# Kernel tuning notes

Hardware: AMD Instinct MI355X
Metric: run time of the kernel (lower is better)

## Reference

```python
import jax, jax.numpy as jnp
import numpy as np

B, F, C, NS, P, N = 256, 2048, 16384, 65536, 8, 32
T, W_BU, W_H, P_MARGIN, N_MARGIN = 1.0, 1.0, 10.0, 0.1, 0.1


def setup_inputs() -> dict:
    key = jax.random.key(0)
    ks = jax.random.split(key, 8)
    inputs = jax.random.normal(ks[0], (B, F), jnp.float32)
    targets = jax.random.randint(ks[1], (B,), 0, C)
    # batch global indices: unique (original .item() assumes a single match)
    indexs = jax.random.permutation(ks[2], NS)[:B].astype(jnp.int64) if False else jax.random.permutation(ks[2], jnp.arange(NS))[:B]
    # positive candidates drawn from in-batch indices so they are found in `indexs`
    pos_sel = jax.random.randint(ks[3], (B, P), 0, B)
    ppairs = indexs[pos_sel]
    # negative candidates: arbitrary global indices (mostly not in batch)
    npairs = jax.random.randint(ks[4], (B, N), 0, NS)
    all_label_to_clusterid = jax.random.randint(ks[5], (NS,), 0, C)
    V = jax.random.normal(ks[6], (C, F), jnp.float32)
    V = V / jnp.linalg.norm(V, axis=1, keepdims=True)  # bank rows are L2-normalized by the update rule
    return {"inputs": inputs, "targets": targets, "ppairs": ppairs, "npairs": npairs,
            "indexs": indexs, "all_label_to_clusterid": all_label_to_clusterid, "V": V, "epoch": 1}


def _forward(inputs, targets, ppairs, npairs, indexs, all_label_to_clusterid, V, epoch):
    # Exclusive branch: logits against the memory bank (V treated as constant)
    outputs = (inputs @ V.T) * T  # [B, C]
    logp = jax.nn.log_softmax(outputs, axis=1)
    bu_loss = -jnp.mean(jnp.take_along_axis(logp, targets[:, None], axis=1))

    # ms_loss (use_prior=True, use_table=True)
    ni = inputs / jnp.linalg.norm(inputs, axis=1, keepdims=True)
    sims = ni @ ni.T          # [B, B]
    tsims = ni @ V.T          # [B, C]

    # positives found in the batch: (ppair == indexs).nonzero()
    mp = ppairs[:, :, None] == indexs[None, None, :]        # [B, P, B]
    found_p = jnp.any(mp, axis=2)
    idx_p = jnp.argmax(mp, axis=2)
    psim_b = jnp.take_along_axis(sims, idx_p, axis=1)       # [B, P]
    mask_pb = found_p & (ppairs >= 0)
    # table positive: tsims[i, target] appended if nonzero
    tp = jnp.take_along_axis(tsims, targets[:, None], axis=1)  # [B, 1]
    mask_tp = tp != 0
    psims = jnp.concatenate([psim_b, tp], axis=1)           # [B, P+1]
    pmask = jnp.concatenate([mask_pb, mask_tp], axis=1)

    # negatives found in the batch
    mn = npairs[:, :, None] == indexs[None, None, :]        # [B, N, B]
    found_n = jnp.any(mn, axis=2)
    idx_n = jnp.argmax(mn, axis=2)
    nsim_b = jnp.take_along_axis(sims, idx_n, axis=1)       # [B, N]
    mask_nb = found_n & (npairs >= 0)
    # table negative appended for EVERY npair (indent level in original): tsims[i, clusterid[npair]]
    ncid = all_label_to_clusterid[jnp.clip(npairs, 0, None)]
    tn = jnp.take_along_axis(tsims, ncid, axis=1)           # [B, N]
    mask_tn = (npairs >= 0) & (tn != 0)
    nsims = jnp.concatenate([nsim_b, tn], axis=1)           # [B, 2N]
    nmask = jnp.concatenate([mask_nb, mask_tn], axis=1)

    # thresholds: max(nsims) or -3 (+p_margin); min(psims) or 3 (-n_margin)
    p_thrd = jnp.where(jnp.any(nmask, 1), jnp.max(jnp.where(nmask, nsims, -jnp.inf), 1), -3.0) + P_MARGIN
    n_thrd = jnp.where(jnp.any(pmask, 1), jnp.min(jnp.where(pmask, psims, jnp.inf), 1), 3.0) - N_MARGIN

    hp = pmask & (psims < p_thrd[:, None])
    hn = nmask & (nsims > n_thrd[:, None]) & (nsims < 0.999999)

    hp_sum = jnp.sum(jnp.where(hp, jnp.exp(-2.0 * (psims - 0.5)), 0.0))
    hn_sum = jnp.sum(jnp.where(hn, jnp.exp(50.0 * (nsims - 0.5)), 0.0))
    hp_loss = jnp.where(jnp.any(hp), 0.5 * jnp.log1p(hp_sum), 0.0)
    hn_loss = jnp.where(jnp.any(hn), (1.0 / 50.0) * jnp.log1p(hn_sum), 0.0)
    # original builds hpsims/hnsims with torch.tensor(...), which DETACHES them
    h_loss = jax.lax.stop_gradient(hp_loss + hn_loss)

    loss = W_BU * bu_loss + W_H * h_loss
    return loss, outputs


def reference(inputs, targets, ppairs, npairs, indexs, all_label_to_clusterid, V, epoch):
    return _forward(inputs, targets, ppairs, npairs, indexs, all_label_to_clusterid, V, epoch)
```

## Files before the change

### kernel.cpp

```cpp
#include <hip/hip_runtime.h>
#include <hip/hip_bf16.h>
#include <math.h>

#define B_SZ 256
#define F_SZ 2048
#define C_SZ 16384
#define P_SZ 8
#define N_SZ 32
#define NTILE 256

typedef __bf16 bf16x8 __attribute__((ext_vector_type(8)));
typedef float f32x4 __attribute__((ext_vector_type(4)));
typedef unsigned short us8 __attribute__((ext_vector_type(8)));

typedef __attribute__((address_space(3))) unsigned int lds_u32;
typedef __attribute__((address_space(1))) const unsigned int glb_u32;

#define WAITCNT_VM4   0x0F74
#define WAITCNT_VM0   0x0F70
#define WAITCNT_LGKM0 0xC07F

__device__ __forceinline__ unsigned short f2bf(float x) {
    union { float f; unsigned int u; } v; v.f = x;
    unsigned int r = v.u + 0x7FFFu + ((v.u >> 16) & 1u);
    return (unsigned short)(r >> 16);
}

__global__ __launch_bounds__(256) void prep_kernel(const float* __restrict__ inputs,
                                                   unsigned short* __restrict__ Abf,
                                                   float* __restrict__ norms) {
    const int row = blockIdx.x;
    const int tid = threadIdx.x;
    const float* rp = inputs + (size_t)row * F_SZ + tid * 8;
    float4 v0 = *(const float4*)(rp);
    float4 v1 = *(const float4*)(rp + 4);
    us8 o;
    o[0]=f2bf(v0.x); o[1]=f2bf(v0.y); o[2]=f2bf(v0.z); o[3]=f2bf(v0.w);
    o[4]=f2bf(v1.x); o[5]=f2bf(v1.y); o[6]=f2bf(v1.z); o[7]=f2bf(v1.w);
    *(us8*)(Abf + (size_t)row * F_SZ + tid * 8) = o;
    float ss = v0.x*v0.x + v0.y*v0.y + v0.z*v0.z + v0.w*v0.w
             + v1.x*v1.x + v1.y*v1.y + v1.z*v1.z + v1.w*v1.w;
    __shared__ float red[256];
    red[tid] = ss; __syncthreads();
    for (int s = 128; s > 0; s >>= 1) { if (tid < s) red[tid] += red[tid+s]; __syncthreads(); }
    if (tid == 0) norms[row] = sqrtf(red[0]);
}

#define BM 128
#define BN 64
#define BK 64
#define BPAD 72
#define KITERS (F_SZ / BK)

__global__ __launch_bounds__(256, 2) void gemm_kernel(const unsigned short* __restrict__ Abf,
                                                      const float* __restrict__ V,
                                                      float* __restrict__ Cout,
                                                      float* __restrict__ pmax,
                                                      float* __restrict__ psum) {
    __shared__ unsigned short As[3][BM * BK];
    __shared__ unsigned short Bs[2][BN * BPAD];
    __shared__ float sm[BM * 2], ss2[BM * 2];

    const int tid = threadIdx.x;
    const int lane = tid & 63;
    const int wid = tid >> 6;
    const int wm = wid >> 1, wn = wid & 1;
    const int q = lane >> 4, l16 = lane & 15;

    const int bid = blockIdx.x;
    const int mhalf = (bid >> 3) & 1;
    const int slab  = (bid & 7) | ((bid >> 4) << 3);
    const int bm0 = mhalf * BM;
    const int bn0 = slab * BN;

    f32x4 acc[4][2];
    #pragma unroll
    for (int i = 0; i < 4; i++)
        #pragma unroll
        for (int j = 0; j < 2; j++) acc[i][j] = (f32x4){0.f, 0.f, 0.f, 0.f};

    const int arow = tid >> 3;
    const int akc = (tid & 7) ^ (arow & 7);
    const unsigned short* AgBase = Abf + (size_t)(bm0 + arow) * F_SZ + akc * 8;

    const int bcol = tid >> 2, bseg = tid & 3;
    const float* BgBase = V + (size_t)(bn0 + bcol) * F_SZ + bseg * 16;
    const int bsoff = bcol * BPAD + bseg * 16;

    float4 b0, b1, b2, b3;

    auto issueA = [&](int ring, int k0) {
        #pragma unroll
        for (int j = 0; j < 4; ++j) {
            __builtin_amdgcn_global_load_lds(
                (glb_u32*)(AgBase + (size_t)j * 32 * F_SZ + k0),
                (lds_u32*)&As[ring][(j * 256 + wid * 64) * 8],
                16, 0, 0);
        }
    };
    auto loadB = [&](int k0) {
        b0 = *(const float4*)(BgBase + k0);
        b1 = *(const float4*)(BgBase + k0 + 4);
        b2 = *(const float4*)(BgBase + k0 + 8);
        b3 = *(const float4*)(BgBase + k0 + 12);
    };
    auto writeB = [&](int buf) {
        us8 w0, w1;
        w0[0]=f2bf(b0.x); w0[1]=f2bf(b0.y); w0[2]=f2bf(b0.z); w0[3]=f2bf(b0.w);
        w0[4]=f2bf(b1.x); w0[5]=f2bf(b1.y); w0[6]=f2bf(b1.z); w0[7]=f2bf(b1.w);
        w1[0]=f2bf(b2.x); w1[1]=f2bf(b2.y); w1[2]=f2bf(b2.z); w1[3]=f2bf(b2.w);
        w1[4]=f2bf(b3.x); w1[5]=f2bf(b3.y); w1[6]=f2bf(b3.z); w1[7]=f2bf(b3.w);
        *(us8*)&Bs[buf][bsoff] = w0;
        *(us8*)&Bs[buf][bsoff + 8] = w1;
    };
    auto compute = [&](int ring, int buf) {
        #pragma unroll
        for (int ks = 0; ks < 2; ++ks) {
            bf16x8 af[4], bfv[2];
            const int kc = ks * 4 + q;
            #pragma unroll
            for (int mi = 0; mi < 4; ++mi) {
                const int row = wm * 64 + mi * 16 + l16;
                af[mi] = *(const bf16x8*)&As[ring][row * 64 + (kc ^ (row & 7)) * 8];
            }
            #pragma unroll
            for (int ni = 0; ni < 2; ++ni) {
                const int col = wn * 32 + ni * 16 + l16;
                bfv[ni] = *(const bf16x8*)&Bs[buf][col * BPAD + ks * 32 + q * 8];
            }
            #pragma unroll
            for (int mi = 0; mi < 4; ++mi)
                #pragma unroll
                for (int ni = 0; ni < 2; ++ni)
                    acc[mi][ni] = __builtin_amdgcn_mfma_f32_16x16x32_bf16(af[mi], bfv[ni], acc[mi][ni], 0, 0, 0);
        }
    };

    issueA(0, 0);
    issueA(1, BK);
    loadB(0);
    __builtin_amdgcn_s_waitcnt(WAITCNT_VM0);
    writeB(0);
    __syncthreads();

    int cur = 0;
    int nxt2 = 2;
    #pragma unroll 1
    for (int it = 0; it < KITERS; ++it) {
        if (it + 1 < KITERS) loadB((it + 1) * BK);
        if (it + 2 < KITERS) issueA(nxt2, (it + 2) * BK);
        compute(cur, it & 1);
        if (it + 2 < KITERS)      __builtin_amdgcn_s_waitcnt(WAITCNT_VM4);
        else if (it + 1 < KITERS) __builtin_amdgcn_s_waitcnt(WAITCNT_VM0);
        if (it + 1 < KITERS) {
            writeB((it + 1) & 1);
            __builtin_amdgcn_s_waitcnt(WAITCNT_LGKM0);
            __builtin_amdgcn_s_barrier();
        }
        cur  = (cur == 2) ? 0 : cur + 1;
        nxt2 = (nxt2 == 2) ? 0 : nxt2 + 1;
    }

    #pragma unroll
    for (int mi = 0; mi < 4; ++mi) {
        const int r0 = bm0 + wm * 64 + mi * 16 + q * 4;
        #pragma unroll
        for (int ni = 0; ni < 2; ++ni) {
            const int c0 = bn0 + wn * 32 + ni * 16 + l16;
            #pragma unroll
            for (int r = 0; r < 4; ++r)
                Cout[(size_t)(r0 + r) * C_SZ + c0] = acc[mi][ni][r];
        }
    }

    #pragma unroll
    for (int mi = 0; mi < 4; ++mi) {
        #pragma unroll
        for (int r = 0; r < 4; ++r) {
            float mloc = fmaxf(acc[mi][0][r], acc[mi][1][r]);
            #pragma unroll
            for (int off = 1; off < 16; off <<= 1)
                mloc = fmaxf(mloc, __shfl_xor(mloc, off, 64));
            float sloc = __expf(acc[mi][0][r] - mloc) + __expf(acc[mi][1][r] - mloc);
            #pragma unroll
            for (int off = 1; off < 16; off <<= 1)
                sloc += __shfl_xor(sloc, off, 64);
            if (l16 == 0) {
                const int lrow = wm * 64 + mi * 16 + q * 4 + r;
                sm[lrow * 2 + wn] = mloc;
                ss2[lrow * 2 + wn] = sloc;
            }
        }
    }
    __syncthreads();
    if (tid < BM) {
        float m1 = sm[tid * 2], s1 = ss2[tid * 2];
        float m2 = sm[tid * 2 + 1], s2 = ss2[tid * 2 + 1];
        float nm = fmaxf(m1, m2);
        float s = s1 * __expf(m1 - nm) + s2 * __expf(m2 - nm);
        pmax[(bm0 + tid) * NTILE + slab] = nm;
        psum[(bm0 + tid) * NTILE + slab] = s;
    }
}

__global__ __launch_bounds__(256) void softmax_combine_kernel(
    const float* __restrict__ pmax, const float* __restrict__ psum,
    const float* __restrict__ outputs, const int* __restrict__ targets,
    float* __restrict__ bu_part)
{
    const int row = blockIdx.x;
    const int tid = threadIdx.x;
    __shared__ float rm[256], rs[256];
    rm[tid] = pmax[row * NTILE + tid];
    rs[tid] = psum[row * NTILE + tid];
    __syncthreads();
    for (int s = 128; s > 0; s >>= 1) {
        if (tid < s) {
            float a = rm[tid], sa = rs[tid];
            float b = rm[tid + s], sb = rs[tid + s];
            float nn = fmaxf(a, b);
            rs[tid] = sa * __expf(a - nn) + sb * __expf(b - nn);
            rm[tid] = nn;
        }
        __syncthreads();
    }
    if (tid == 0) {
        float logZ = rm[0] + logf(rs[0]);
        bu_part[row] = -(outputs[(size_t)row * C_SZ + targets[row]] - logZ);
    }
}

__global__ __launch_bounds__(256) void pairs_kernel(
    const float* __restrict__ inputs, const int* __restrict__ targets,
    const int* __restrict__ ppairs, const int* __restrict__ npairs,
    const int* __restrict__ indexs, const int* __restrict__ cluster,
    const float* __restrict__ outputs, const float* __restrict__ norms,
    float* __restrict__ hp_part, float* __restrict__ hn_part,
    int* __restrict__ flag_part)
{
    const int i = blockIdx.x;
    const int tid = threadIdx.x;
    __shared__ int idxbuf[B_SZ];
    __shared__ int pj[P_SZ];
    __shared__ int nj[N_SZ];
    __shared__ float simp[P_SZ];
    __shared__ float simn[N_SZ];
    __shared__ float tnv[N_SZ];
    __shared__ float s_tp;

    idxbuf[tid] = indexs[tid];
    __syncthreads();

    const float* row = outputs + (size_t)i * C_SZ;
    const float ni_norm = norms[i];

    if (tid < P_SZ) {
        int pp = ppairs[i * P_SZ + tid];
        int f = -1;
        if (pp >= 0) for (int j = 0; j < B_SZ; j++) if (idxbuf[j] == pp) { f = j; break; }
        pj[tid] = f;
    } else if (tid < P_SZ + N_SZ) {
        int t = tid - P_SZ;
        int np = npairs[i * N_SZ + t];
        int f = -1;
        if (np >= 0) for (int j = 0; j < B_SZ; j++) if (idxbuf[j] == np) { f = j; break; }
        nj[t] = f;
        int cid = cluster[np < 0 ? 0 : np];
        tnv[t] = row[cid] / ni_norm;
    }
    if (tid == P_SZ + N_SZ) s_tp = row[targets[i]] / ni_norm;
    __syncthreads();

    const int lane = tid & 63, wv = tid >> 6;
    for (int qq = wv; qq < P_SZ + N_SZ; qq += 4) {
        int j = (qq < P_SZ) ? pj[qq] : nj[qq - P_SZ];
        float s = 0.f;
        if (j >= 0) {
            const float* xi = inputs + (size_t)i * F_SZ;
            const float* xj = inputs + (size_t)j * F_SZ;
            float d = 0.f;
            for (int k = lane; k < F_SZ; k += 64) d += xi[k] * xj[k];
            for (int off = 32; off > 0; off >>= 1) d += __shfl_down(d, off);
            s = d / (ni_norm * norms[j]);
        }
        if (lane == 0) { if (qq < P_SZ) simp[qq] = s; else simn[qq - P_SZ] = s; }
    }
    __syncthreads();

    if (tid == 0) {
        float psims[P_SZ + 1]; bool pmask[P_SZ + 1];
        for (int p = 0; p < P_SZ; p++) {
            int pp = ppairs[i * P_SZ + p];
            pmask[p] = (pj[p] >= 0) && (pp >= 0);
            psims[p] = simp[p];
        }
        psims[P_SZ] = s_tp; pmask[P_SZ] = (s_tp != 0.0f);

        float nsims[2 * N_SZ]; bool nmask[2 * N_SZ];
        for (int t = 0; t < N_SZ; t++) {
            int np = npairs[i * N_SZ + t];
            nmask[t] = (nj[t] >= 0) && (np >= 0);
            nsims[t] = simn[t];
            nsims[N_SZ + t] = tnv[t];
            nmask[N_SZ + t] = (np >= 0) && (tnv[t] != 0.0f);
        }
        bool anyp = false, anyn = false;
        float maxn = -INFINITY, minp = INFINITY;
        for (int t = 0; t < 2 * N_SZ; t++) if (nmask[t]) { anyn = true; maxn = fmaxf(maxn, nsims[t]); }
        for (int p = 0; p < P_SZ + 1; p++) if (pmask[p]) { anyp = true; minp = fminf(minp, psims[p]); }
        float p_thrd = (anyn ? maxn : -3.0f) + 0.1f;
        float n_thrd = (anyp ? minp : 3.0f) - 0.1f;
        float hps = 0.f, hns = 0.f; int fl = 0;
        for (int p = 0; p < P_SZ + 1; p++)
            if (pmask[p] && psims[p] < p_thrd) { fl |= 1; hps += expf(-2.0f * (psims[p] - 0.5f)); }
        for (int t = 0; t < 2 * N_SZ; t++)
            if (nmask[t] && nsims[t] > n_thrd && nsims[t] < 0.999999f) { fl |= 2; hns += expf(50.0f * (nsims[t] - 0.5f)); }
        hp_part[i] = hps; hn_part[i] = hns; flag_part[i] = fl;
    }
}

__global__ __launch_bounds__(256) void finalize_kernel(
    const float* __restrict__ bu_part, const float* __restrict__ hp_part,
    const float* __restrict__ hn_part, const int* __restrict__ flag_part,
    float* __restrict__ d_out)
{
    __shared__ float r1[256], r2[256], r3[256];
    __shared__ int rf[256];
    const int tid = threadIdx.x;
    r1[tid] = bu_part[tid]; r2[tid] = hp_part[tid]; r3[tid] = hn_part[tid]; rf[tid] = flag_part[tid];
    __syncthreads();
    for (int s = 128; s > 0; s >>= 1) {
        if (tid < s) { r1[tid] += r1[tid+s]; r2[tid] += r2[tid+s]; r3[tid] += r3[tid+s]; rf[tid] |= rf[tid+s]; }
        __syncthreads();
    }
    if (tid == 0) {
        float bu = r1[0] / (float)B_SZ;
        float hp_loss = (rf[0] & 1) ? 0.5f * log1pf(r2[0]) : 0.0f;
        float hn_loss = (rf[0] & 2) ? (1.0f / 50.0f) * log1pf(r3[0]) : 0.0f;
        d_out[0] = 1.0f * bu + 10.0f * (hp_loss + hn_loss);
    }
}

extern "C" void kernel_launch(void* const* d_in, const int* in_sizes, int n_in,
                              void* d_out, int out_size, void* d_ws, size_t ws_size,
                              hipStream_t stream) {
    const float* inputs  = (const float*)d_in[0];
    const int*   targets = (const int*)d_in[1];
    const int*   ppairs  = (const int*)d_in[2];
    const int*   npairs  = (const int*)d_in[3];
    const int*   indexs  = (const int*)d_in[4];
    const int*   cluster = (const int*)d_in[5];
    const float* V       = (const float*)d_in[6];
    float* out = (float*)d_out;

    char* ws = (char*)d_ws;
    unsigned short* Abf = (unsigned short*)ws;
    float* norms   = (float*)(ws + (size_t)B_SZ * F_SZ * 2);
    float* bu_part = norms + B_SZ;
    float* hp_part = bu_part + B_SZ;
    float* hn_part = hp_part + B_SZ;
    int*   flag_part = (int*)(hn_part + B_SZ);
    float* pmax = (float*)(flag_part + B_SZ);
    float* psum = pmax + (size_t)B_SZ * NTILE;

    prep_kernel<<<B_SZ, 256, 0, stream>>>(inputs, Abf, norms);
    gemm_kernel<<<512, 256, 0, stream>>>(Abf, V, out + 1, pmax, psum);
    softmax_combine_kernel<<<B_SZ, 256, 0, stream>>>(pmax, psum, out + 1, targets, bu_part);
    pairs_kernel<<<B_SZ, 256, 0, stream>>>(inputs, targets, ppairs, npairs, indexs,
                                           cluster, out + 1, norms,
                                           hp_part, hn_part, flag_part);
    finalize_kernel<<<1, 256, 0, stream>>>(bu_part, hp_part, hn_part, flag_part, out);
}
```

Before: 302.7 us.

## Deepen B prefetch to two stages and fuse softmax combine into pairs kernel

The GEMM's fp32 V loads now go into two alternating register sets, so the load for k-step it+2 is issued two iterations ahead. The wait count is relaxed to allow 8 outstanding loads, which hides more global latency behind the MFMA work. The separate softmax_combine kernel is removed and its log-sum-exp reduction is folded into pairs_kernel, saving one launch. The cost is more live registers in the GEMM, which could reduce occupancy, plus extra shared memory and barriers in pairs_kernel.

```diff
diff --git a/kernel.cpp b/kernel.cpp
--- a/kernel.cpp
+++ b/kernel.cpp
@@ -16,7 +16,7 @@
 typedef __attribute__((address_space(3))) unsigned int lds_u32;
 typedef __attribute__((address_space(1))) const unsigned int glb_u32;
 
-#define WAITCNT_VM4   0x0F74
+#define WAITCNT_VM8   0x0F78
 #define WAITCNT_VM0   0x0F70
 #define WAITCNT_LGKM0 0xC07F
 
@@ -87,7 +87,8 @@
     const float* BgBase = V + (size_t)(bn0 + bcol) * F_SZ + bseg * 16;
     const int bsoff = bcol * BPAD + bseg * 16;
 
-    float4 b0, b1, b2, b3;
+    float4 p0, p1, p2, p3;
+    float4 q0, q1, q2, q3;
 
     auto issueA = [&](int ring, int k0) {
         #pragma unroll
@@ -98,20 +99,35 @@
                 16, 0, 0);
         }
     };
-    auto loadB = [&](int k0) {
-        b0 = *(const float4*)(BgBase + k0);
-        b1 = *(const float4*)(BgBase + k0 + 4);
-        b2 = *(const float4*)(BgBase + k0 + 8);
-        b3 = *(const float4*)(BgBase + k0 + 12);
-    };
-    auto writeB = [&](int buf) {
+    auto loadBp = [&](int k0) {
+        p0 = *(const float4*)(BgBase + k0);
+        p1 = *(const float4*)(BgBase + k0 + 4);
+        p2 = *(const float4*)(BgBase + k0 + 8);
+        p3 = *(const float4*)(BgBase + k0 + 12);
+    };
+    auto loadBq = [&](int k0) {
+        q0 = *(const float4*)(BgBase + k0);
+        q1 = *(const float4*)(BgBase + k0 + 4);
+        q2 = *(const float4*)(BgBase + k0 + 8);
+        q3 = *(const float4*)(BgBase + k0 + 12);
+    };
+    auto writeBp = [&]() {
         us8 w0, w1;
-        w0[0]=f2bf(b0.x); w0[1]=f2bf(b0.y); w0[2]=f2bf(b0.z); w0[3]=f2bf(b0.w);
-        w0[4]=f2bf(b1.x); w0[5]=f2bf(b1.y); w0[6]=f2bf(b1.z); w0[7]=f2bf(b1.w);
-        w1[0]=f2bf(b2.x); w1[1]=f2bf(b2.y); w1[2]=f2bf(b2.z); w1[3]=f2bf(b2.w);
-        w1[4]=f2bf(b3.x); w1[5]=f2bf(b3.y); w1[6]=f2bf(b3.z); w1[7]=f2bf(b3.w);
-        *(us8*)&Bs[buf][bsoff] = w0;
-        *(us8*)&Bs[buf][bsoff + 8] = w1;
+        w0[0]=f2bf(p0.x); w0[1]=f2bf(p0.y); w0[2]=f2bf(p0.z); w0[3]=f2bf(p0.w);
+        w0[4]=f2bf(p1.x); w0[5]=f2bf(p1.y); w0[6]=f2bf(p1.z); w0[7]=f2bf(p1.w);
+        w1[0]=f2bf(p2.x); w1[1]=f2bf(p2.y); w1[2]=f2bf(p2.z); w1[3]=f2bf(p2.w);
+        w1[4]=f2bf(p3.x); w1[5]=f2bf(p3.y); w1[6]=f2bf(p3.z); w1[7]=f2bf(p3.w);
+        *(us8*)&Bs[0][bsoff] = w0;
+        *(us8*)&Bs[0][bsoff + 8] = w1;
+    };
+    auto writeBq = [&]() {
+        us8 w0, w1;
+        w0[0]=f2bf(q0.x); w0[1]=f2bf(q0.y); w0[2]=f2bf(q0.z); w0[3]=f2bf(q0.w);
+        w0[4]=f2bf(q1.x); w0[5]=f2bf(q1.y); w0[6]=f2bf(q1.z); w0[7]=f2bf(q1.w);
+        w1[0]=f2bf(q2.x); w1[1]=f2bf(q2.y); w1[2]=f2bf(q2.z); w1[3]=f2bf(q2.w);
+        w1[4]=f2bf(q3.x); w1[5]=f2bf(q3.y); w1[6]=f2bf(q3.z); w1[7]=f2bf(q3.w);
+        *(us8*)&Bs[1][bsoff] = w0;
+        *(us8*)&Bs[1][bsoff + 8] = w1;
     };
     auto compute = [&](int ring, int buf) {
         #pragma unroll
@@ -137,23 +153,29 @@
     };
 
     issueA(0, 0);
+    loadBp(0);
     issueA(1, BK);
-    loadB(0);
-    __builtin_amdgcn_s_waitcnt(WAITCNT_VM0);
-    writeB(0);
-    __syncthreads();
+    loadBq(BK);
+    __builtin_amdgcn_s_waitcnt(WAITCNT_VM8);
+    writeBp();
+    __builtin_amdgcn_s_waitcnt(WAITCNT_LGKM0);
+    __builtin_amdgcn_s_barrier();
 
     int cur = 0;
     int nxt2 = 2;
     #pragma unroll 1
     for (int it = 0; it < KITERS; ++it) {
-        if (it + 1 < KITERS) loadB((it + 1) * BK);
-        if (it + 2 < KITERS) issueA(nxt2, (it + 2) * BK);
+        if (it + 2 < KITERS) {
+            issueA(nxt2, (it + 2) * BK);
+            if (!(it & 1)) loadBp((it + 2) * BK);
+            else           loadBq((it + 2) * BK);
+        }
         compute(cur, it & 1);
-        if (it + 2 < KITERS)      __builtin_amdgcn_s_waitcnt(WAITCNT_VM4);
+        if (it + 2 < KITERS)      __builtin_amdgcn_s_waitcnt(WAITCNT_VM8);
         else if (it + 1 < KITERS) __builtin_amdgcn_s_waitcnt(WAITCNT_VM0);
         if (it + 1 < KITERS) {
-            writeB((it + 1) & 1);
+            if (!(it & 1)) writeBq();
+            else           writeBp();
             __builtin_amdgcn_s_waitcnt(WAITCNT_LGKM0);
             __builtin_amdgcn_s_barrier();
         }
@@ -203,38 +225,13 @@
     }
 }
 
-__global__ __launch_bounds__(256) void softmax_combine_kernel(
-    const float* __restrict__ pmax, const float* __restrict__ psum,
-    const float* __restrict__ outputs, const int* __restrict__ targets,
-    float* __restrict__ bu_part)
-{
-    const int row = blockIdx.x;
-    const int tid = threadIdx.x;
-    __shared__ float rm[256], rs[256];
-    rm[tid] = pmax[row * NTILE + tid];
-    rs[tid] = psum[row * NTILE + tid];
-    __syncthreads();
-    for (int s = 128; s > 0; s >>= 1) {
-        if (tid < s) {
-            float a = rm[tid], sa = rs[tid];
-            float b = rm[tid + s], sb = rs[tid + s];
-            float nn = fmaxf(a, b);
-            rs[tid] = sa * __expf(a - nn) + sb * __expf(b - nn);
-            rm[tid] = nn;
-        }
-        __syncthreads();
-    }
-    if (tid == 0) {
-        float logZ = rm[0] + logf(rs[0]);
-        bu_part[row] = -(outputs[(size_t)row * C_SZ + targets[row]] - logZ);
-    }
-}
-
 __global__ __launch_bounds__(256) void pairs_kernel(
     const float* __restrict__ inputs, const int* __restrict__ targets,
     const int* __restrict__ ppairs, const int* __restrict__ npairs,
     const int* __restrict__ indexs, const int* __restrict__ cluster,
     const float* __restrict__ outputs, const float* __restrict__ norms,
+    const float* __restrict__ pmax, const float* __restrict__ psum,
+    float* __restrict__ bu_part,
     float* __restrict__ hp_part, float* __restrict__ hn_part,
     int* __restrict__ flag_part)
 {
@@ -247,12 +244,30 @@
     __shared__ float simn[N_SZ];
     __shared__ float tnv[N_SZ];
     __shared__ float s_tp;
+    __shared__ float rm[256], rs[256];
 
     idxbuf[tid] = indexs[tid];
-    __syncthreads();
+    rm[tid] = pmax[i * NTILE + tid];
+    rs[tid] = psum[i * NTILE + tid];
+    __syncthreads();
+    for (int s = 128; s > 0; s >>= 1) {
+        if (tid < s) {
+            float a = rm[tid], sa = rs[tid];
+            float b = rm[tid + s], sb = rs[tid + s];
+            float nn = fmaxf(a, b);
+            rs[tid] = sa * __expf(a - nn) + sb * __expf(b - nn);
+            rm[tid] = nn;
+        }
+        __syncthreads();
+    }
 
     const float* row = outputs + (size_t)i * C_SZ;
     const float ni_norm = norms[i];
+
+    if (tid == 0) {
+        float logZ = rm[0] + logf(rs[0]);
+        bu_part[i] = -(row[targets[i]] - logZ);
+    }
 
     if (tid < P_SZ) {
         int pp = ppairs[i * P_SZ + tid];
@@ -365,9 +380,8 @@
 
     prep_kernel<<<B_SZ, 256, 0, stream>>>(inputs, Abf, norms);
     gemm_kernel<<<512, 256, 0, stream>>>(Abf, V, out + 1, pmax, psum);
-    softmax_combine_kernel<<<B_SZ, 256, 0, stream>>>(pmax, psum, out + 1, targets, bu_part);
     pairs_kernel<<<B_SZ, 256, 0, stream>>>(inputs, targets, ppairs, npairs, indexs,
-                                           cluster, out + 1, norms,
-                                           hp_part, hn_part, flag_part);
+                                           cluster, out + 1, norms, pmax, psum,
+                                           bu_part, hp_part, hn_part, flag_part);
     finalize_kernel<<<1, 256, 0, stream>>>(bu_part, hp_part, hn_part, flag_part, out);
 }
```

Result: no change. 300.1 us (-0.9%).

## Pre-convert V to bf16 and stream both GEMM operands via direct LDS loads

Applied to the files above, without the earlier changes.

Adds a bulk fp32-to-bf16 conversion of the memory bank V in the prep kernel, so the GEMM can load both A and B tiles with asynchronous global-to-LDS loads into a triple-buffered swizzled ring. This removes the register staging, in-loop conversion and extra LDS writes for B. The softmax-combine kernel is merged into the pairs kernel to drop a launch. The cost is an extra full pass over V that reads fp32 and writes bf16 each call, plus more workspace.

```diff
diff --git a/kernel.cpp b/kernel.cpp
--- a/kernel.cpp
+++ b/kernel.cpp
@@ -16,9 +16,8 @@
 typedef __attribute__((address_space(3))) unsigned int lds_u32;
 typedef __attribute__((address_space(1))) const unsigned int glb_u32;
 
-#define WAITCNT_VM4   0x0F74
+#define WAITCNT_VM6   0x0F76
 #define WAITCNT_VM0   0x0F70
-#define WAITCNT_LGKM0 0xC07F
 
 __device__ __forceinline__ unsigned short f2bf(float x) {
     union { float f; unsigned int u; } v; v.f = x;
@@ -26,11 +25,29 @@
     return (unsigned short)(r >> 16);
 }
 
+#define VCONV_BLKS 4096
+
 __global__ __launch_bounds__(256) void prep_kernel(const float* __restrict__ inputs,
+                                                   const float* __restrict__ V,
                                                    unsigned short* __restrict__ Abf,
+                                                   unsigned short* __restrict__ Vbf,
                                                    float* __restrict__ norms) {
-    const int row = blockIdx.x;
     const int tid = threadIdx.x;
+    if (blockIdx.x < VCONV_BLKS) {
+        const size_t base = (size_t)blockIdx.x * 8192 + tid * 8;
+        #pragma unroll
+        for (int c = 0; c < 4; ++c) {
+            const float* rp = V + base + c * 2048;
+            float4 v0 = *(const float4*)(rp);
+            float4 v1 = *(const float4*)(rp + 4);
+            us8 o;
+            o[0]=f2bf(v0.x); o[1]=f2bf(v0.y); o[2]=f2bf(v0.z); o[3]=f2bf(v0.w);
+            o[4]=f2bf(v1.x); o[5]=f2bf(v1.y); o[6]=f2bf(v1.z); o[7]=f2bf(v1.w);
+            *(us8*)(Vbf + base + c * 2048) = o;
+        }
+        return;
+    }
+    const int row = blockIdx.x - VCONV_BLKS;
     const float* rp = inputs + (size_t)row * F_SZ + tid * 8;
     float4 v0 = *(const float4*)(rp);
     float4 v1 = *(const float4*)(rp + 4);
@@ -49,16 +66,15 @@
 #define BM 128
 #define BN 64
 #define BK 64
-#define BPAD 72
 #define KITERS (F_SZ / BK)
 
 __global__ __launch_bounds__(256, 2) void gemm_kernel(const unsigned short* __restrict__ Abf,
-                                                      const float* __restrict__ V,
+                                                      const unsigned short* __restrict__ Vbf,
                                                       float* __restrict__ Cout,
                                                       float* __restrict__ pmax,
                                                       float* __restrict__ psum) {
     __shared__ unsigned short As[3][BM * BK];
-    __shared__ unsigned short Bs[2][BN * BPAD];
+    __shared__ unsigned short Bs[3][BN * BK];
     __shared__ float sm[BM * 2], ss2[BM * 2];
 
     const int tid = threadIdx.x;
@@ -79,17 +95,12 @@
         #pragma unroll
         for (int j = 0; j < 2; j++) acc[i][j] = (f32x4){0.f, 0.f, 0.f, 0.f};
 
-    const int arow = tid >> 3;
-    const int akc = (tid & 7) ^ (arow & 7);
-    const unsigned short* AgBase = Abf + (size_t)(bm0 + arow) * F_SZ + akc * 8;
-
-    const int bcol = tid >> 2, bseg = tid & 3;
-    const float* BgBase = V + (size_t)(bn0 + bcol) * F_SZ + bseg * 16;
-    const int bsoff = bcol * BPAD + bseg * 16;
-
-    float4 b0, b1, b2, b3;
-
-    auto issueA = [&](int ring, int k0) {
+    const int srow = tid >> 3;
+    const int skc = (tid & 7) ^ (srow & 7);
+    const unsigned short* AgBase = Abf + (size_t)(bm0 + srow) * F_SZ + skc * 8;
+    const unsigned short* BgBase = Vbf + (size_t)(bn0 + srow) * F_SZ + skc * 8;
+
+    auto issueTile = [&](int ring, int k0) {
         #pragma unroll
         for (int j = 0; j < 4; ++j) {
             __builtin_amdgcn_global_load_lds(
@@ -97,23 +108,15 @@
                 (lds_u32*)&As[ring][(j * 256 + wid * 64) * 8],
                 16, 0, 0);
         }
+        #pragma unroll
+        for (int j = 0; j < 2; ++j) {
+            __builtin_amdgcn_global_load_lds(
+                (glb_u32*)(BgBase + (size_t)j * 32 * F_SZ + k0),
+                (lds_u32*)&Bs[ring][(j * 256 + wid * 64) * 8],
+                16, 0, 0);
+        }
     };
-    auto loadB = [&](int k0) {
-        b0 = *(const float4*)(BgBase + k0);
-        b1 = *(const float4*)(BgBase + k0 + 4);
-        b2 = *(const float4*)(BgBase + k0 + 8);
-        b3 = *(const float4*)(BgBase + k0 + 12);
-    };
-    auto writeB = [&](int buf) {
-        us8 w0, w1;
-        w0[0]=f2bf(b0.x); w0[1]=f2bf(b0.y); w0[2]=f2bf(b0.z); w0[3]=f2bf(b0.w);
-        w0[4]=f2bf(b1.x); w0[5]=f2bf(b1.y); w0[6]=f2bf(b1.z); w0[7]=f2bf(b1.w);
-        w1[0]=f2bf(b2.x); w1[1]=f2bf(b2.y); w1[2]=f2bf(b2.z); w1[3]=f2bf(b2.w);
-        w1[4]=f2bf(b3.x); w1[5]=f2bf(b3.y); w1[6]=f2bf(b3.z); w1[7]=f2bf(b3.w);
-        *(us8*)&Bs[buf][bsoff] = w0;
-        *(us8*)&Bs[buf][bsoff + 8] = w1;
-    };
-    auto compute = [&](int ring, int buf) {
+    auto compute = [&](int ring) {
         #pragma unroll
         for (int ks = 0; ks < 2; ++ks) {
             bf16x8 af[4], bfv[2];
@@ -126,7 +129,7 @@
             #pragma unroll
             for (int ni = 0; ni < 2; ++ni) {
                 const int col = wn * 32 + ni * 16 + l16;
-                bfv[ni] = *(const bf16x8*)&Bs[buf][col * BPAD + ks * 32 + q * 8];
+                bfv[ni] = *(const bf16x8*)&Bs[ring][col * 64 + (kc ^ (col & 7)) * 8];
             }
             #pragma unroll
             for (int mi = 0; mi < 4; ++mi)
@@ -136,27 +139,20 @@
         }
     };
 
-    issueA(0, 0);
-    issueA(1, BK);
-    loadB(0);
-    __builtin_amdgcn_s_waitcnt(WAITCNT_VM0);
-    writeB(0);
-    __syncthreads();
+    issueTile(0, 0);
+    issueTile(1, BK);
+    __builtin_amdgcn_s_waitcnt(WAITCNT_VM6);
+    __builtin_amdgcn_s_barrier();
 
     int cur = 0;
     int nxt2 = 2;
     #pragma unroll 1
     for (int it = 0; it < KITERS; ++it) {
-        if (it + 1 < KITERS) loadB((it + 1) * BK);
-        if (it + 2 < KITERS) issueA(nxt2, (it + 2) * BK);
-        compute(cur, it & 1);
-        if (it + 2 < KITERS)      __builtin_amdgcn_s_waitcnt(WAITCNT_VM4);
+        if (it + 2 < KITERS) issueTile(nxt2, (it + 2) * BK);
+        compute(cur);
+        if (it + 2 < KITERS)      __builtin_amdgcn_s_waitcnt(WAITCNT_VM6);
         else if (it + 1 < KITERS) __builtin_amdgcn_s_waitcnt(WAITCNT_VM0);
-        if (it + 1 < KITERS) {
-            writeB((it + 1) & 1);
-            __builtin_amdgcn_s_waitcnt(WAITCNT_LGKM0);
-            __builtin_amdgcn_s_barrier();
-        }
+        if (it + 1 < KITERS) __builtin_amdgcn_s_barrier();
         cur  = (cur == 2) ? 0 : cur + 1;
         nxt2 = (nxt2 == 2) ? 0 : nxt2 + 1;
     }
@@ -203,38 +199,13 @@
     }
 }
 
-__global__ __launch_bounds__(256) void softmax_combine_kernel(
-    const float* __restrict__ pmax, const float* __restrict__ psum,
-    const float* __restrict__ outputs, const int* __restrict__ targets,
-    float* __restrict__ bu_part)
-{
-    const int row = blockIdx.x;
-    const int tid = threadIdx.x;
-    __shared__ float rm[256], rs[256];
-    rm[tid] = pmax[row * NTILE + tid];
-    rs[tid] = psum[row * NTILE + tid];
-    __syncthreads();
-    for (int s = 128; s > 0; s >>= 1) {
-        if (tid < s) {
-            float a = rm[tid], sa = rs[tid];
-            float b = rm[tid + s], sb = rs[tid + s];
-            float nn = fmaxf(a, b);
-            rs[tid] = sa * __expf(a - nn) + sb * __expf(b - nn);
-            rm[tid] = nn;
-        }
-        __syncthreads();
-    }
-    if (tid == 0) {
-        float logZ = rm[0] + logf(rs[0]);
-        bu_part[row] = -(outputs[(size_t)row * C_SZ + targets[row]] - logZ);
-    }
-}
-
 __global__ __launch_bounds__(256) void pairs_kernel(
     const float* __restrict__ inputs, const int* __restrict__ targets,
     const int* __restrict__ ppairs, const int* __restrict__ npairs,
     const int* __restrict__ indexs, const int* __restrict__ cluster,
     const float* __restrict__ outputs, const float* __restrict__ norms,
+    const float* __restrict__ pmax, const float* __restrict__ psum,
+    float* __restrict__ bu_part,
     float* __restrict__ hp_part, float* __restrict__ hn_part,
     int* __restrict__ flag_part)
 {
@@ -247,12 +218,30 @@
     __shared__ float simn[N_SZ];
     __shared__ float tnv[N_SZ];
     __shared__ float s_tp;
+    __shared__ float rm[256], rs[256];
 
     idxbuf[tid] = indexs[tid];
-    __syncthreads();
+    rm[tid] = pmax[i * NTILE + tid];
+    rs[tid] = psum[i * NTILE + tid];
+    __syncthreads();
+    for (int s = 128; s > 0; s >>= 1) {
+        if (tid < s) {
+            float a = rm[tid], sa = rs[tid];
+            float b = rm[tid + s], sb = rs[tid + s];
+            float nn = fmaxf(a, b);
+            rs[tid] = sa * __expf(a - nn) + sb * __expf(b - nn);
+            rm[tid] = nn;
+        }
+        __syncthreads();
+    }
 
     const float* row = outputs + (size_t)i * C_SZ;
     const float ni_norm = norms[i];
+
+    if (tid == 0) {
+        float logZ = rm[0] + logf(rs[0]);
+        bu_part[i] = -(row[targets[i]] - logZ);
+    }
 
     if (tid < P_SZ) {
         int pp = ppairs[i * P_SZ + tid];
@@ -354,8 +343,9 @@
     float* out = (float*)d_out;
 
     char* ws = (char*)d_ws;
-    unsigned short* Abf = (unsigned short*)ws;
-    float* norms   = (float*)(ws + (size_t)B_SZ * F_SZ * 2);
+    unsigned short* Vbf = (unsigned short*)ws;
+    unsigned short* Abf = Vbf + (size_t)C_SZ * F_SZ;
+    float* norms   = (float*)(Abf + (size_t)B_SZ * F_SZ);
     float* bu_part = norms + B_SZ;
     float* hp_part = bu_part + B_SZ;
     float* hn_part = hp_part + B_SZ;
@@ -363,11 +353,10 @@
     float* pmax = (float*)(flag_part + B_SZ);
     float* psum = pmax + (size_t)B_SZ * NTILE;
 
-    prep_kernel<<<B_SZ, 256, 0, stream>>>(inputs, Abf, norms);
-    gemm_kernel<<<512, 256, 0, stream>>>(Abf, V, out + 1, pmax, psum);
-    softmax_combine_kernel<<<B_SZ, 256, 0, stream>>>(pmax, psum, out + 1, targets, bu_part);
+    prep_kernel<<<VCONV_BLKS + B_SZ, 256, 0, stream>>>(inputs, V, Abf, Vbf, norms);
+    gemm_kernel<<<512, 256, 0, stream>>>(Abf, Vbf, out + 1, pmax, psum);
     pairs_kernel<<<B_SZ, 256, 0, stream>>>(inputs, targets, ppairs, npairs, indexs,
-                                           cluster, out + 1, norms,
-                                           hp_part, hn_part, flag_part);
+                                           cluster, out + 1, norms, pmax, psum,
+                                           bu_part, hp_part, hn_part, flag_part);
     finalize_kernel<<<1, 256, 0, stream>>>(bu_part, hp_part, hn_part, flag_part, out);
 }
```

After: 326.0 us. +7.7%, slower.

## Cover all batch rows per GEMM block and fold softmax combine into pairs

Applied to the files above, without the earlier changes.

The GEMM block tile grows from 128 to all 256 batch rows, with 512 threads and one block per 64-column slab of V. Each fp32 V slab is now loaded and converted to bf16 once rather than once per M-half. The separate softmax_combine kernel is removed and its log-sum-exp reduction moved into pairs_kernel, saving a launch. In exchange the grid is only 256 blocks at one block per CU with a larger LDS footprint, which reduces latency hiding.

```diff
diff --git a/kernel.cpp b/kernel.cpp
--- a/kernel.cpp
+++ b/kernel.cpp
@@ -46,13 +46,13 @@
     if (tid == 0) norms[row] = sqrtf(red[0]);
 }
 
-#define BM 128
+#define BM 256
 #define BN 64
 #define BK 64
 #define BPAD 72
 #define KITERS (F_SZ / BK)
 
-__global__ __launch_bounds__(256, 2) void gemm_kernel(const unsigned short* __restrict__ Abf,
+__global__ __launch_bounds__(512, 1) void gemm_kernel(const unsigned short* __restrict__ Abf,
                                                       const float* __restrict__ V,
                                                       float* __restrict__ Cout,
                                                       float* __restrict__ pmax,
@@ -67,10 +67,7 @@
     const int wm = wid >> 1, wn = wid & 1;
     const int q = lane >> 4, l16 = lane & 15;
 
-    const int bid = blockIdx.x;
-    const int mhalf = (bid >> 3) & 1;
-    const int slab  = (bid & 7) | ((bid >> 4) << 3);
-    const int bm0 = mhalf * BM;
+    const int slab = blockIdx.x;
     const int bn0 = slab * BN;
 
     f32x4 acc[4][2];
@@ -79,39 +76,34 @@
         #pragma unroll
         for (int j = 0; j < 2; j++) acc[i][j] = (f32x4){0.f, 0.f, 0.f, 0.f};
 
-    const int arow = tid >> 3;
-    const int akc = (tid & 7) ^ (arow & 7);
-    const unsigned short* AgBase = Abf + (size_t)(bm0 + arow) * F_SZ + akc * 8;
-
-    const int bcol = tid >> 2, bseg = tid & 3;
-    const float* BgBase = V + (size_t)(bn0 + bcol) * F_SZ + bseg * 16;
-    const int bsoff = bcol * BPAD + bseg * 16;
-
-    float4 b0, b1, b2, b3;
+    const int srow = tid >> 3;
+    const int skc = (tid & 7) ^ (srow & 7);
+    const unsigned short* AgBase = Abf + (size_t)srow * F_SZ + skc * 8;
+
+    const int bcol = tid >> 3, bseg = tid & 7;
+    const float* BgBase = V + (size_t)(bn0 + bcol) * F_SZ + bseg * 8;
+    const int bsoff = bcol * BPAD + bseg * 8;
+
+    float4 b0, b1;
 
     auto issueA = [&](int ring, int k0) {
         #pragma unroll
         for (int j = 0; j < 4; ++j) {
             __builtin_amdgcn_global_load_lds(
-                (glb_u32*)(AgBase + (size_t)j * 32 * F_SZ + k0),
-                (lds_u32*)&As[ring][(j * 256 + wid * 64) * 8],
+                (glb_u32*)(AgBase + (size_t)j * 64 * F_SZ + k0),
+                (lds_u32*)&As[ring][(j * 512 + tid) * 8],
                 16, 0, 0);
         }
     };
     auto loadB = [&](int k0) {
         b0 = *(const float4*)(BgBase + k0);
         b1 = *(const float4*)(BgBase + k0 + 4);
-        b2 = *(const float4*)(BgBase + k0 + 8);
-        b3 = *(const float4*)(BgBase + k0 + 12);
     };
     auto writeB = [&](int buf) {
-        us8 w0, w1;
-        w0[0]=f2bf(b0.x); w0[1]=f2bf(b0.y); w0[2]=f2bf(b0.z); w0[3]=f2bf(b0.w);
-        w0[4]=f2bf(b1.x); w0[5]=f2bf(b1.y); w0[6]=f2bf(b1.z); w0[7]=f2bf(b1.w);
-        w1[0]=f2bf(b2.x); w1[1]=f2bf(b2.y); w1[2]=f2bf(b2.z); w1[3]=f2bf(b2.w);
-        w1[4]=f2bf(b3.x); w1[5]=f2bf(b3.y); w1[6]=f2bf(b3.z); w1[7]=f2bf(b3.w);
-        *(us8*)&Bs[buf][bsoff] = w0;
-        *(us8*)&Bs[buf][bsoff + 8] = w1;
+        us8 w;
+        w[0]=f2bf(b0.x); w[1]=f2bf(b0.y); w[2]=f2bf(b0.z); w[3]=f2bf(b0.w);
+        w[4]=f2bf(b1.x); w[5]=f2bf(b1.y); w[6]=f2bf(b1.z); w[7]=f2bf(b1.w);
+        *(us8*)&Bs[buf][bsoff] = w;
     };
     auto compute = [&](int ring, int buf) {
         #pragma unroll
@@ -137,11 +129,12 @@
     };
 
     issueA(0, 0);
+    loadB(0);
     issueA(1, BK);
-    loadB(0);
-    __builtin_amdgcn_s_waitcnt(WAITCNT_VM0);
+    __builtin_amdgcn_s_waitcnt(WAITCNT_VM4);
     writeB(0);
-    __syncthreads();
+    __builtin_amdgcn_s_waitcnt(WAITCNT_LGKM0);
+    __builtin_amdgcn_s_barrier();
 
     int cur = 0;
     int nxt2 = 2;
@@ -163,7 +156,7 @@
 
     #pragma unroll
     for (int mi = 0; mi < 4; ++mi) {
-        const int r0 = bm0 + wm * 64 + mi * 16 + q * 4;
+        const int r0 = wm * 64 + mi * 16 + q * 4;
         #pragma unroll
         for (int ni = 0; ni < 2; ++ni) {
             const int c0 = bn0 + wn * 32 + ni * 16 + l16;
@@ -198,35 +191,8 @@
         float m2 = sm[tid * 2 + 1], s2 = ss2[tid * 2 + 1];
         float nm = fmaxf(m1, m2);
         float s = s1 * __expf(m1 - nm) + s2 * __expf(m2 - nm);
-        pmax[(bm0 + tid) * NTILE + slab] = nm;
-        psum[(bm0 + tid) * NTILE + slab] = s;
-    }
-}
-
-__global__ __launch_bounds__(256) void softmax_combine_kernel(
-    const float* __restrict__ pmax, const float* __restrict__ psum,
-    const float* __restrict__ outputs, const int* __restrict__ targets,
-    float* __restrict__ bu_part)
-{
-    const int row = blockIdx.x;
-    const int tid = threadIdx.x;
-    __shared__ float rm[256], rs[256];
-    rm[tid] = pmax[row * NTILE + tid];
-    rs[tid] = psum[row * NTILE + tid];
-    __syncthreads();
-    for (int s = 128; s > 0; s >>= 1) {
-        if (tid < s) {
-            float a = rm[tid], sa = rs[tid];
-            float b = rm[tid + s], sb = rs[tid + s];
-            float nn = fmaxf(a, b);
-            rs[tid] = sa * __expf(a - nn) + sb * __expf(b - nn);
-            rm[tid] = nn;
-        }
-        __syncthreads();
-    }
-    if (tid == 0) {
-        float logZ = rm[0] + logf(rs[0]);
-        bu_part[row] = -(outputs[(size_t)row * C_SZ + targets[row]] - logZ);
+        pmax[tid * NTILE + slab] = nm;
+        psum[tid * NTILE + slab] = s;
     }
 }
 
@@ -235,6 +201,8 @@
     const int* __restrict__ ppairs, const int* __restrict__ npairs,
     const int* __restrict__ indexs, const int* __restrict__ cluster,
     const float* __restrict__ outputs, const float* __restrict__ norms,
+    const float* __restrict__ pmax, const float* __restrict__ psum,
+    float* __restrict__ bu_part,
     float* __restrict__ hp_part, float* __restrict__ hn_part,
     int* __restrict__ flag_part)
 {
@@ -247,12 +215,30 @@
     __shared__ float simn[N_SZ];
     __shared__ float tnv[N_SZ];
     __shared__ float s_tp;
+    __shared__ float rm[256], rs[256];
 
     idxbuf[tid] = indexs[tid];
-    __syncthreads();
+    rm[tid] = pmax[i * NTILE + tid];
+    rs[tid] = psum[i * NTILE + tid];
+    __syncthreads();
+    for (int s = 128; s > 0; s >>= 1) {
+        if (tid < s) {
+            float a = rm[tid], sa = rs[tid];
+            float b = rm[tid + s], sb = rs[tid + s];
+            float nn = fmaxf(a, b);
+            rs[tid] = sa * __expf(a - nn) + sb * __expf(b - nn);
+            rm[tid] = nn;
+        }
+        __syncthreads();
+    }
 
     const float* row = outputs + (size_t)i * C_SZ;
     const float ni_norm = norms[i];
+
+    if (tid == 0) {
+        float logZ = rm[0] + logf(rs[0]);
+        bu_part[i] = -(row[targets[i]] - logZ);
+    }
 
     if (tid < P_SZ) {
         int pp = ppairs[i * P_SZ + tid];
@@ -364,10 +350,9 @@
     float* psum = pmax + (size_t)B_SZ * NTILE;
 
     prep_kernel<<<B_SZ, 256, 0, stream>>>(inputs, Abf, norms);
-    gemm_kernel<<<512, 256, 0, stream>>>(Abf, V, out + 1, pmax, psum);
-    softmax_combine_kernel<<<B_SZ, 256, 0, stream>>>(pmax, psum, out + 1, targets, bu_part);
+    gemm_kernel<<<256, 512, 0, stream>>>(Abf, V, out + 1, pmax, psum);
     pairs_kernel<<<B_SZ, 256, 0, stream>>>(inputs, targets, ppairs, npairs, indexs,
-                                           cluster, out + 1, norms,
-                                           hp_part, hn_part, flag_part);
+                                           cluster, out + 1, norms, pmax, psum,
+                                           bu_part, hp_part, hn_part, flag_part);
     finalize_kernel<<<1, 256, 0, stream>>>(bu_part, hp_part, hn_part, flag_part, out);
 }
```

Result: no change. 301.3 us (median of 2 runs) (-0.5%).
